# Kernel optimization log

Measured on AMD Instinct MI355X. Metric: run time of the kernel, lower is better.

## Reference

```python
import jax, jax.numpy as jnp
import numpy as np

D_MODEL = 2048
NUM_HEADS = 32
NUM_KV_HEADS = 8
HEAD_DIM = D_MODEL // NUM_HEADS  # 64
B, S = 2, 2048


def rotary_cos_sin(seq_len, head_dim, dtype=jnp.float32):
    inv_freq = 1.0 / (10000.0 ** (jnp.arange(0, head_dim, 2, dtype=jnp.float32) / head_dim))
    t = jnp.arange(seq_len, dtype=jnp.float32)
    freqs = t[:, None] * inv_freq[None, :]          # [S, hd/2]
    emb = jnp.concatenate([freqs, freqs], axis=-1)  # [S, hd]
    return emb.astype(dtype).reshape(1, seq_len, 1, head_dim), None  # placeholder


def apply_rotary_emb(x, cos, sin):
    # faithful to source: interleaved rotate-half, concatenated cos/sin
    x1 = x[..., ::2]
    x2 = x[..., 1::2]
    rotated = jnp.stack([-x2, x1], axis=-1).reshape(x.shape)
    return x * cos + rotated * sin


def setup_inputs() -> dict:
    key = jax.random.key(0)
    ks = jax.random.split(key, 5)
    sc = 0.02
    x = jax.random.normal(ks[0], (B, S, D_MODEL), dtype=jnp.float32)
    Wq = jax.random.normal(ks[1], (D_MODEL, D_MODEL), dtype=jnp.float32) * sc
    Wk = jax.random.normal(ks[2], (D_MODEL, NUM_KV_HEADS * HEAD_DIM), dtype=jnp.float32) * sc
    Wv = jax.random.normal(ks[3], (D_MODEL, NUM_KV_HEADS * HEAD_DIM), dtype=jnp.float32) * sc
    Wo = jax.random.normal(ks[4], (D_MODEL, D_MODEL), dtype=jnp.float32) * sc
    mask = jnp.tril(jnp.ones((S, S), dtype=jnp.int32))[None, None]  # [1,1,S,S] causal
    return {"x": x, "mask": mask, "Wq": Wq, "Wk": Wk, "Wv": Wv, "Wo": Wo}


def reference(x, mask, Wq, Wk, Wv, Wo):
    b, s, _ = x.shape
    q = (x @ Wq).reshape(b, s, NUM_HEADS, HEAD_DIM)
    k = (x @ Wk).reshape(b, s, NUM_KV_HEADS, HEAD_DIM)
    v = (x @ Wv).reshape(b, s, NUM_KV_HEADS, HEAD_DIM)

    inv_freq = 1.0 / (10000.0 ** (jnp.arange(0, HEAD_DIM, 2, dtype=jnp.float32) / HEAD_DIM))
    t = jnp.arange(s, dtype=jnp.float32)
    freqs = t[:, None] * inv_freq[None, :]
    emb = jnp.concatenate([freqs, freqs], axis=-1)         # [S, hd]
    cos = jnp.cos(emb)[None, :, None, :].astype(x.dtype)   # [1,S,1,hd]
    sin = jnp.sin(emb)[None, :, None, :].astype(x.dtype)

    q = apply_rotary_emb(q, cos, sin)
    k = apply_rotary_emb(k, cos, sin)

    rep = NUM_HEADS // NUM_KV_HEADS
    k = jnp.repeat(k, rep, axis=2)  # [B,S,H,hd]
    v = jnp.repeat(v, rep, axis=2)

    q = q.transpose(0, 2, 1, 3)  # [B,H,S,hd]
    k = k.transpose(0, 2, 1, 3)
    v = v.transpose(0, 2, 1, 3)

    scale = 1.0 / jnp.sqrt(jnp.asarray(HEAD_DIM, dtype=x.dtype))
    scores = jnp.einsum('bhqd,bhkd->bhqk', q, k) * scale
    scores = jnp.where(mask == 0, jnp.asarray(-jnp.inf, scores.dtype), scores)
    attn = jax.nn.softmax(scores, axis=-1)
    out = jnp.einsum('bhqk,bhkd->bhqd', attn, v)
    out = out.transpose(0, 2, 1, 3).reshape(b, s, D_MODEL)
    return out @ Wo
```

## Files before the change

### kernel.cpp

```cpp
#include <hip/hip_runtime.h>
#include <hip/hip_bf16.h>

typedef __bf16 bf16;
typedef __bf16 bf16x8 __attribute__((ext_vector_type(8)));
typedef float  f32x4  __attribute__((ext_vector_type(4)));

#define B_  2
#define S_  2048
#define H_  32
#define HK_ 8
#define D_  64
#define DM_ 2048
#define LDQ 3072

__device__ __forceinline__ void async_copy16(const bf16* g, bf16* l) {
    __builtin_amdgcn_global_load_lds((const __attribute__((address_space(1))) void*)g,
                                     (__attribute__((address_space(3))) void*)l,
                                     16, 0, 0);
}

__global__ __launch_bounds__(256) void convert_x(const float* __restrict__ in,
                                                 bf16* __restrict__ out) {
    const long i = (long)blockIdx.x * 256 + threadIdx.x;
    const float4 v = ((const float4*)in)[i];
    bf16* o = out + i * 4;
    o[0] = (bf16)v.x; o[1] = (bf16)v.y; o[2] = (bf16)v.z; o[3] = (bf16)v.w;
}

__global__ __launch_bounds__(256) void transpose2d(const float* __restrict__ in,
                                                   bf16* __restrict__ out,
                                                   int R, int C) {
    __shared__ bf16 tile[32][33];
    const int tx = threadIdx.x & 31;
    const int ty = threadIdx.x >> 5;
    const long r0 = (long)blockIdx.y * 32;
    const long c0 = (long)blockIdx.x * 32;
#pragma unroll
    for (int k = 0; k < 4; ++k)
        tile[ty + 8 * k][tx] = (bf16)in[(r0 + ty + 8 * k) * C + c0 + tx];
    __syncthreads();
#pragma unroll
    for (int k = 0; k < 4; ++k)
        out[(c0 + ty + 8 * k) * R + r0 + tx] = tile[tx][ty + 8 * k];
}

__global__ __launch_bounds__(256) void v_transpose(const bf16* __restrict__ qkv,
                                                   bf16* __restrict__ out) {
    __shared__ bf16 tile[32][33];
    const int p = blockIdx.z;
    const int b = p >> 3, h = p & 7;
    const int s0 = blockIdx.x * 32;
    const int d0 = blockIdx.y * 32;
    const int tx = threadIdx.x & 31;
    const int ty = threadIdx.x >> 5;
    const bf16* ip = qkv + (long)(b * S_) * LDQ + 2560 + h * 64;
#pragma unroll
    for (int k = 0; k < 4; ++k)
        tile[ty + 8 * k][tx] = ip[(long)(s0 + ty + 8 * k) * LDQ + d0 + tx];
    __syncthreads();
    bf16* op = out + ((long)(b * HK_ + h) * D_) * S_;
#pragma unroll
    for (int k = 0; k < 4; ++k)
        op[(long)(d0 + ty + 8 * k) * S_ + s0 + tx] = tile[tx][ty + 8 * k];
}

__global__ __launch_bounds__(256) void rope_all(bf16* qkv) {
    const int idx = blockIdx.x * 256 + threadIdx.x;
    const int i  = idx & 31;
    const int s  = (idx >> 5) & (S_ - 1);
    const int ord = idx >> 16;
    const int b  = (ord >= 40) ? 1 : 0;
    const int hh = ord - 40 * b;
    const int colOff = (hh < 32) ? hh * 64 : 2048 + (hh - 32) * 64;
    const long base = (long)(b * S_ + s) * LDQ + colOff;
    const float x0 = (float)qkv[base + 2 * i];
    const float x1 = (float)qkv[base + 2 * i + 1];
    const float t = (float)s;
    const float c10k = 9.210340371976184f;
    const int i0 = (2 * i) & 31;
    const int i1 = (2 * i + 1) & 31;
    const float f0 = t * expf(-(float)i0 * (c10k / 32.f));
    const float f1 = t * expf(-(float)i1 * (c10k / 32.f));
    const float o0 = x0 * cosf(f0) - x1 * sinf(f0);
    const float o1 = x1 * cosf(f1) + x0 * sinf(f1);
    qkv[base + 2 * i]     = (bf16)o0;
    qkv[base + 2 * i + 1] = (bf16)o1;
}

template <typename OutT>
__global__ __launch_bounds__(256, 3) void gemm_tb(const bf16* __restrict__ A, int lda,
                                                  const bf16* __restrict__ Bt, int ldb,
                                                  OutT* __restrict__ C, int ldc, int K) {
    constexpr int ABUF = 128 * 32;
    constexpr int BUF  = 2 * ABUF;
    __shared__ __align__(16) bf16 lds[3 * BUF];

    const int tid  = threadIdx.x;
    const int w    = tid >> 6;
    const int lane = tid & 63;
    const int quad = lane >> 4;
    const int l16  = lane & 15;
    const int wr   = w >> 1;
    const int wc   = w & 1;
    const long m0  = (long)blockIdx.y * 128;
    const long n0  = (long)blockIdx.x * 128;

    const int srow = lane >> 2;
    const int schk = ((lane & 3) ^ ((lane >> 3) & 3)) * 8;
    const bf16* Ag = A  + (m0 + w * 32 + srow) * lda + schk;
    const bf16* Bg = Bt + (n0 + w * 32 + srow) * ldb + schk;

    const int rchk = (quad ^ ((l16 >> 1) & 3)) * 8;
    const int aoff = (wr * 64 + l16) * 32 + rchk;
    const int boff = (wc * 64 + l16) * 32 + rchk;

#define STAGE(buf, k0)                                                          \
    do {                                                                        \
        async_copy16(Ag + (k0),            (buf) + (w * 32) * 32);              \
        async_copy16(Ag + 16 * lda + (k0), (buf) + (w * 32 + 16) * 32);         \
        async_copy16(Bg + (k0),            (buf) + ABUF + (w * 32) * 32);       \
        async_copy16(Bg + 16 * ldb + (k0), (buf) + ABUF + (w * 32 + 16) * 32);  \
    } while (0)

    bf16* p0 = lds;
    bf16* p1 = lds + BUF;
    bf16* p2 = lds + 2 * BUF;

    STAGE(p0, 0);
    STAGE(p1, 32);

    f32x4 acc[4][4] = {};
    const int nt = K / 32;

    for (int t = 0; t < nt; ++t) {
        if (t < nt - 1) { asm volatile("s_waitcnt vmcnt(4)" ::: "memory"); }
        else            { asm volatile("s_waitcnt vmcnt(0)" ::: "memory"); }
        __builtin_amdgcn_s_barrier();
        __builtin_amdgcn_sched_barrier(0);
        if (t + 2 < nt) STAGE(p2, (t + 2) * 32);
        bf16x8 a[4], b[4];
#pragma unroll
        for (int m = 0; m < 4; ++m) a[m] = *(const bf16x8*)(p0 + aoff + m * 16 * 32);
#pragma unroll
        for (int n = 0; n < 4; ++n) b[n] = *(const bf16x8*)(p0 + ABUF + boff + n * 16 * 32);
        asm volatile("s_waitcnt lgkmcnt(0)" ::: "memory");
        __builtin_amdgcn_sched_barrier(0);
        __builtin_amdgcn_s_setprio(1);
#pragma unroll
        for (int m = 0; m < 4; ++m)
#pragma unroll
            for (int n = 0; n < 4; ++n)
                acc[m][n] = __builtin_amdgcn_mfma_f32_16x16x32_bf16(a[m], b[n], acc[m][n], 0, 0, 0);
        __builtin_amdgcn_s_setprio(0);
        bf16* tp = p0; p0 = p1; p1 = p2; p2 = tp;
    }
#undef STAGE

#pragma unroll
    for (int m = 0; m < 4; ++m) {
        const long r = m0 + wr * 64 + m * 16 + quad * 4;
#pragma unroll
        for (int n = 0; n < 4; ++n) {
            const long c = n0 + wc * 64 + n * 16 + l16;
#pragma unroll
            for (int reg = 0; reg < 4; ++reg)
                C[(r + reg) * ldc + c] = (OutT)acc[m][n][reg];
        }
    }
}

__global__ __launch_bounds__(256, 4) void attn_fused(bf16* qkv,
                                                     const bf16* __restrict__ Vt) {
    __shared__ __align__(16) bf16 Ks[64 * 64];
    __shared__ __align__(16) bf16 Vs[64 * 64];
    __shared__ __align__(16) bf16 Pbuf[4][32 * 72];
    const int tid  = threadIdx.x;
    const int w    = tid >> 6;
    const int lane = tid & 63;
    const int quad = lane >> 4;
    const int l16  = lane & 15;
    const int r8   = lane >> 3;
    const int sw   = (lane & 7) ^ r8;
    const int x7   = l16 & 7;

    const int bid = blockIdx.x;
    const int grp = bid & 15;
    const int qi  = 63 - (bid >> 4);
    const int hk  = grp & 7;
    const int b   = grp >> 3;
    const int h   = hk * 4 + w;

    const bf16* kp = qkv + (long)(b * S_) * LDQ + 2048 + hk * 64;
    const bf16* vp = Vt + (long)(b * HK_ + hk) * D_ * S_;
    bf16* P = &Pbuf[w][0];

    const float C1 = 0.18033688011112043f;
    const float C2 = 23.083120654223415f;
    const f32x4 zero = {0.f, 0.f, 0.f, 0.f};

    const int q0 = qi * 32;
    bf16* qp = qkv + (long)(b * S_ + q0) * LDQ + h * 64;

    bf16x8 aq[2][2];
#pragma unroll
    for (int i = 0; i < 2; ++i)
#pragma unroll
        for (int half = 0; half < 2; ++half)
            aq[i][half] = *(const bf16x8*)(qp + (long)(i * 16 + l16) * LDQ + half * 32 + quad * 8);

    f32x4 accO[2][4] = {};
    float ps[2][4] = {};

    const int nkt = q0 / 64 + 1;
    for (int kt = 0; kt < nkt; ++kt) {
        const int kb = kt * 64;
        __syncthreads();
#pragma unroll
        for (int t = 0; t < 2; ++t) {
            const int rloc = w * 16 + t * 8;
            async_copy16(kp + (long)(kb + rloc + r8) * LDQ + sw * 8, Ks + rloc * 64);
            async_copy16(vp + (long)(rloc + r8) * S_ + kb + sw * 8,  Vs + rloc * 64);
        }
        __syncthreads();

        const bool lastTile = (kt == nkt - 1);
#pragma unroll
        for (int g = 0; g < 4; ++g) {
            const int krow = g * 16 + l16;
            const bf16x8 bk0 = *(const bf16x8*)(Ks + krow * 64 + ((quad ^ x7) * 8));
            const bf16x8 bk1 = *(const bf16x8*)(Ks + krow * 64 + (((quad + 4) ^ x7) * 8));
#pragma unroll
            for (int i = 0; i < 2; ++i) {
                __builtin_amdgcn_s_setprio(1);
                f32x4 t = __builtin_amdgcn_mfma_f32_16x16x32_bf16(aq[i][0], bk0, zero, 0, 0, 0);
                f32x4 s = __builtin_amdgcn_mfma_f32_16x16x32_bf16(aq[i][1], bk1, t, 0, 0, 0);
                __builtin_amdgcn_s_setprio(0);
#pragma unroll
                for (int rg = 0; rg < 4; ++rg) {
                    float e;
                    if (lastTile) {
                        const int key  = kb + g * 16 + l16;
                        const int qrow = q0 + i * 16 + quad * 4 + rg;
                        e = (key <= qrow)
                          ? __builtin_amdgcn_exp2f(fminf(s[rg] * C1 - C2, 10.f)) : 0.f;
                    } else {
                        e = __builtin_amdgcn_exp2f(fminf(s[rg] * C1 - C2, 10.f));
                    }
                    ps[i][rg] += e;
                    P[(i * 16 + quad * 4 + rg) * 72 + g * 16 + l16] = (bf16)e;
                }
            }
        }
        __asm__ volatile("s_waitcnt lgkmcnt(0)" ::: "memory");
#pragma unroll
        for (int i = 0; i < 2; ++i) {
            const bf16x8 aP0 = *(const bf16x8*)(P + (i * 16 + l16) * 72 + quad * 8);
            const bf16x8 aP1 = *(const bf16x8*)(P + (i * 16 + l16) * 72 + 32 + quad * 8);
#pragma unroll
            for (int c = 0; c < 4; ++c) {
                const int vrow = c * 16 + l16;
                const bf16x8 bv0 = *(const bf16x8*)(Vs + vrow * 64 + ((quad ^ x7) * 8));
                const bf16x8 bv1 = *(const bf16x8*)(Vs + vrow * 64 + (((quad + 4) ^ x7) * 8));
                __builtin_amdgcn_s_setprio(1);
                accO[i][c] = __builtin_amdgcn_mfma_f32_16x16x32_bf16(aP0, bv0, accO[i][c], 0, 0, 0);
                accO[i][c] = __builtin_amdgcn_mfma_f32_16x16x32_bf16(aP1, bv1, accO[i][c], 0, 0, 0);
                __builtin_amdgcn_s_setprio(0);
            }
        }
        __asm__ volatile("s_waitcnt lgkmcnt(0)" ::: "memory");
    }

#pragma unroll
    for (int off = 1; off < 16; off <<= 1)
#pragma unroll
        for (int i = 0; i < 2; ++i)
#pragma unroll
            for (int rg = 0; rg < 4; ++rg)
                ps[i][rg] += __shfl_xor(ps[i][rg], off, 64);
    float invl[2][4];
#pragma unroll
    for (int i = 0; i < 2; ++i)
#pragma unroll
        for (int rg = 0; rg < 4; ++rg) invl[i][rg] = 1.f / ps[i][rg];

#pragma unroll
    for (int i = 0; i < 2; ++i)
#pragma unroll
        for (int c = 0; c < 4; ++c)
#pragma unroll
            for (int rg = 0; rg < 4; ++rg) {
                const long row = (long)(b * S_ + q0 + i * 16 + quad * 4 + rg);
                qkv[row * LDQ + h * 64 + c * 16 + l16] = (bf16)(accO[i][c][rg] * invl[i][rg]);
            }
}

extern "C" void kernel_launch(void* const* d_in, const int* in_sizes, int n_in,
                              void* d_out, int out_size, void* d_ws, size_t ws_size,
                              hipStream_t stream) {
    (void)in_sizes; (void)n_in; (void)out_size; (void)ws_size;
    const float* x  = (const float*)d_in[0];
    const float* Wq = (const float*)d_in[2];
    const float* Wk = (const float*)d_in[3];
    const float* Wv = (const float*)d_in[4];
    const float* Wo = (const float*)d_in[5];
    float* out = (float*)d_out;

    bf16* qkv = (bf16*)d_ws;
    bf16* wT3 = qkv + 4096L * 3072;
    bf16* xb  = (bf16*)d_out;
    bf16* vT  = xb + 4096L * 2048;

    const dim3 blk(256);

    convert_x<<<dim3(8388608 / (256 * 4)), blk, 0, stream>>>(x, xb);

    transpose2d<<<dim3(64, 64), blk, 0, stream>>>(Wq, wT3, 2048, 2048);
    transpose2d<<<dim3(16, 64), blk, 0, stream>>>(Wk, wT3 + 2048L * 2048, 2048, 512);
    transpose2d<<<dim3(16, 64), blk, 0, stream>>>(Wv, wT3 + 2560L * 2048, 2048, 512);

    gemm_tb<bf16><<<dim3(24, 32), blk, 0, stream>>>(
        xb, 2048, wT3, 2048, qkv, LDQ, 2048);

    rope_all<<<dim3((B_ * (H_ + HK_) * S_ * 32) / 256), blk, 0, stream>>>(qkv);
    v_transpose<<<dim3(S_ / 32, D_ / 32, B_ * HK_), blk, 0, stream>>>(qkv, vT);

    attn_fused<<<dim3(B_ * HK_ * 64), blk, 0, stream>>>(qkv, vT);

    transpose2d<<<dim3(64, 64), blk, 0, stream>>>(Wo, wT3, 2048, 2048);
    gemm_tb<float><<<dim3(16, 32), blk, 0, stream>>>(
        qkv, LDQ, wT3, 2048, out, 2048, 2048);
}
```

Measured before the change: 318.5 us.

## Load K and V fragments directly from global memory, drop LDS staging

```diff
diff --git a/kernel.cpp b/kernel.cpp
--- a/kernel.cpp
+++ b/kernel.cpp
@@ -169,19 +169,15 @@
     }
 }
 
+#define PLD 76
 __global__ __launch_bounds__(256, 4) void attn_fused(bf16* qkv,
                                                      const bf16* __restrict__ Vt) {
-    __shared__ __align__(16) bf16 Ks[64 * 64];
-    __shared__ __align__(16) bf16 Vs[64 * 64];
-    __shared__ __align__(16) bf16 Pbuf[4][32 * 72];
+    __shared__ __align__(16) bf16 Pbuf[4][32 * PLD];
     const int tid  = threadIdx.x;
     const int w    = tid >> 6;
     const int lane = tid & 63;
     const int quad = lane >> 4;
     const int l16  = lane & 15;
-    const int r8   = lane >> 3;
-    const int sw   = (lane & 7) ^ r8;
-    const int x7   = l16 & 7;
 
     const int bid = blockIdx.x;
     const int grp = bid & 15;
@@ -214,21 +210,20 @@
     const int nkt = q0 / 64 + 1;
     for (int kt = 0; kt < nkt; ++kt) {
         const int kb = kt * 64;
-        __syncthreads();
-#pragma unroll
-        for (int t = 0; t < 2; ++t) {
-            const int rloc = w * 16 + t * 8;
-            async_copy16(kp + (long)(kb + rloc + r8) * LDQ + sw * 8, Ks + rloc * 64);
-            async_copy16(vp + (long)(rloc + r8) * S_ + kb + sw * 8,  Vs + rloc * 64);
-        }
-        __syncthreads();
-
         const bool lastTile = (kt == nkt - 1);
+
+        bf16x8 bv[4][2];
+#pragma unroll
+        for (int c = 0; c < 4; ++c)
+#pragma unroll
+            for (int half = 0; half < 2; ++half)
+                bv[c][half] = *(const bf16x8*)(vp + (long)(c * 16 + l16) * S_ + kb + half * 32 + quad * 8);
+
 #pragma unroll
         for (int g = 0; g < 4; ++g) {
-            const int krow = g * 16 + l16;
-            const bf16x8 bk0 = *(const bf16x8*)(Ks + krow * 64 + ((quad ^ x7) * 8));
-            const bf16x8 bk1 = *(const bf16x8*)(Ks + krow * 64 + (((quad + 4) ^ x7) * 8));
+            const long krow = kb + g * 16 + l16;
+            const bf16x8 bk0 = *(const bf16x8*)(kp + krow * LDQ + quad * 8);
+            const bf16x8 bk1 = *(const bf16x8*)(kp + krow * LDQ + 32 + quad * 8);
 #pragma unroll
             for (int i = 0; i < 2; ++i) {
                 __builtin_amdgcn_s_setprio(1);
@@ -247,25 +242,22 @@
                         e = __builtin_amdgcn_exp2f(fminf(s[rg] * C1 - C2, 10.f));
                     }
                     ps[i][rg] += e;
-                    P[(i * 16 + quad * 4 + rg) * 72 + g * 16 + l16] = (bf16)e;
+                    P[(i * 16 + quad * 4 + rg) * PLD + g * 16 + l16] = (bf16)e;
                 }
             }
         }
         __asm__ volatile("s_waitcnt lgkmcnt(0)" ::: "memory");
 #pragma unroll
         for (int i = 0; i < 2; ++i) {
-            const bf16x8 aP0 = *(const bf16x8*)(P + (i * 16 + l16) * 72 + quad * 8);
-            const bf16x8 aP1 = *(const bf16x8*)(P + (i * 16 + l16) * 72 + 32 + quad * 8);
+            const bf16x8 aP0 = *(const bf16x8*)(P + (i * 16 + l16) * PLD + quad * 8);
+            const bf16x8 aP1 = *(const bf16x8*)(P + (i * 16 + l16) * PLD + 32 + quad * 8);
+            __builtin_amdgcn_s_setprio(1);
 #pragma unroll
             for (int c = 0; c < 4; ++c) {
-                const int vrow = c * 16 + l16;
-                const bf16x8 bv0 = *(const bf16x8*)(Vs + vrow * 64 + ((quad ^ x7) * 8));
-                const bf16x8 bv1 = *(const bf16x8*)(Vs + vrow * 64 + (((quad + 4) ^ x7) * 8));
-                __builtin_amdgcn_s_setprio(1);
-                accO[i][c] = __builtin_amdgcn_mfma_f32_16x16x32_bf16(aP0, bv0, accO[i][c], 0, 0, 0);
-                accO[i][c] = __builtin_amdgcn_mfma_f32_16x16x32_bf16(aP1, bv1, accO[i][c], 0, 0, 0);
-                __builtin_amdgcn_s_setprio(0);
+                accO[i][c] = __builtin_amdgcn_mfma_f32_16x16x32_bf16(aP0, bv[c][0], accO[i][c], 0, 0, 0);
+                accO[i][c] = __builtin_amdgcn_mfma_f32_16x16x32_bf16(aP1, bv[c][1], accO[i][c], 0, 0, 0);
             }
+            __builtin_amdgcn_s_setprio(0);
         }
         __asm__ volatile("s_waitcnt lgkmcnt(0)" ::: "memory");
     }
```

After: 420.8 us. 1.32x slower.
